# Kernel optimization log

Hardware: AMD Instinct MI355X
Metric: run time of the kernel (lower is better)

## Reference

```python
import jax, jax.numpy as jnp
import numpy as np

ROPE_THETA = 10000.0
N_KV_HEADS = 8


def _rope(x, pos, theta):
    # x: [..., D] with interleaved (even, odd) rotation pairs; pos: scalar position
    D = x.shape[-1]
    freqs = theta ** (-jnp.arange(0, D, 2, dtype=jnp.float32) / D)  # [D/2]
    ang = pos * freqs
    cos, sin = jnp.cos(ang), jnp.sin(ang)
    x1, x2 = x[..., 0::2], x[..., 1::2]
    return jnp.stack([x1 * cos - x2 * sin, x1 * sin + x2 * cos], axis=-1).reshape(x.shape)


def setup_inputs() -> dict:
    key = jax.random.key(0)
    ks = jax.random.split(key, 5)
    B, DIM, CACHE_LEN, HD = 32, 4096, 4096, 128
    N_HEADS = 32
    qkv_out = (N_HEADS + 2 * N_KV_HEADS) * HD  # 6144
    return {
        "x": jax.random.normal(ks[0], (B, DIM), dtype=jnp.float32),
        "cache_k": jax.random.normal(ks[1], (B, CACHE_LEN, N_KV_HEADS, HD), dtype=jnp.float32),
        "cache_v": jax.random.normal(ks[2], (B, CACHE_LEN, N_KV_HEADS, HD), dtype=jnp.float32),
        "wqkv": jax.random.normal(ks[3], (qkv_out, DIM), dtype=jnp.float32) * 0.02,
        "wo": jax.random.normal(ks[4], (DIM, DIM), dtype=jnp.float32) * 0.02,
        "ctx_len": 4095,
    }


def reference(x, cache_k, cache_v, wqkv, wo, ctx_len):
    B = x.shape[0]
    n_kv = cache_k.shape[2]
    hd = cache_k.shape[3]
    n_heads = (wqkv.shape[0] - 2 * n_kv * hd) // hd
    hpg = n_heads // n_kv  # heads per kv group

    # fused QKV projection
    xqkv = x @ wqkv.T  # [B, (n_heads + 2*n_kv)*hd]
    nq = n_heads * hd
    nk = n_kv * hd
    q = xqkv[:, :nq].reshape(B, n_kv, hpg, hd)
    k = xqkv[:, nq:nq + nk].reshape(B, n_kv, hd)
    v = xqkv[:, nq + nk:].reshape(B, n_kv, hd)

    # rope fused with KV-cache write: new token at position ctx_len
    q = _rope(q, ctx_len, ROPE_THETA)
    k = _rope(k, ctx_len, ROPE_THETA)
    cache_k = cache_k.at[:, ctx_len].set(k)
    cache_v = cache_v.at[:, ctx_len].set(v)

    T = ctx_len + 1  # valid cache length (python int -> static slice)
    K = cache_k[:, :T]  # [B, T, n_kv, hd]
    V = cache_v[:, :T]

    # GQA attention: q [b, g, h, d], K/V [b, t, g, d]
    scores = jnp.einsum("bghd,btgd->bght", q, K) / jnp.sqrt(jnp.float32(hd))
    w = jax.nn.softmax(scores, axis=-1)
    o = jnp.einsum("bght,btgd->bghd", w, V).reshape(B, n_heads * hd)
    return o @ wo.T
```

## Files before the change

kernel.cpp:

```cpp
#include <hip/hip_runtime.h>
#include <math.h>

#define BATCH 32
#define DIM   4096
#define CLEN  4096
#define HD    128
#define NKV   8
#define NHEAD 32
#define QKVN  6144
#define KVSTR (NKV * HD)
#define GN    64
#define KSEG  128
#define KSTG  4
#define KTOT  512
#define NSEG  8
#define NCH   16
#define TC    256
#define NSLOT 16
#define MNEG  -1.0e30f
#define SMASK -3.0e38f

template <int CTRL>
__device__ __forceinline__ float dpp_add(float x) {
  int y = __builtin_amdgcn_update_dpp(0, __float_as_int(x), CTRL, 0xF, 0xF, true);
  return x + __int_as_float(y);
}

__device__ __forceinline__ float half_reduce(float s) {
  s = dpp_add<0xB1>(s);
  s = dpp_add<0x4E>(s);
  s = dpp_add<0x124>(s);
  s = dpp_add<0x128>(s);
  s += __int_as_float(__builtin_amdgcn_ds_swizzle(__float_as_int(s), 0x401F));
  return s;
}

__device__ __forceinline__ float xhalf32(float v, int lane) {
  return __int_as_float(__builtin_amdgcn_ds_bpermute((lane ^ 32) << 2, __float_as_int(v)));
}

__global__ __launch_bounds__(256)
void gemm_partial(const float* __restrict__ X, const float* __restrict__ W,
                  float* __restrict__ part, const int N) {
  __shared__ float xs[KSEG * 32];
  __shared__ float wl[KSEG * 64];
  const int tid = threadIdx.x;
  const int c   = tid & 31;
  const int r   = tid >> 5;
  const int cx7 = c & 7;
  const int n0  = blockIdx.x * GN;
  const int k00 = blockIdx.y * KTOT;
  const int bq8 = tid & 7;
  const int tq  = tid >> 3;
  const int nqq = tq >> 1;
  const int nqo = (tq & 1) << 1;

  float a00=0,a01=0, a10=0,a11=0, a20=0,a21=0, a30=0,a31=0;

  float* xwp  = xs + (c * 4) * 32 + ((r ^ cx7) << 2);
  float* wwp0 = wl + (c * 4) * 64 + ((r ^ cx7) << 2);
  float* wwp1 = wwp0 + 32;

  for (int kk = 0; kk < KSTG; ++kk) {
    const int k0 = k00 + kk * KSEG;
    const float* Xp = X + (size_t)(r * 4) * DIM + k0 + c * 4;
    const float4 xv0 = *(const float4*)(Xp);
    const float4 xv1 = *(const float4*)(Xp + DIM);
    const float4 xv2 = *(const float4*)(Xp + 2 * DIM);
    const float4 xv3 = *(const float4*)(Xp + 3 * DIM);
    const float* Wp0 = W + (size_t)(n0 + r * 4) * DIM + k0 + c * 4;
    const float4 wv00 = *(const float4*)(Wp0);
    const float4 wv01 = *(const float4*)(Wp0 + DIM);
    const float4 wv02 = *(const float4*)(Wp0 + 2 * DIM);
    const float4 wv03 = *(const float4*)(Wp0 + 3 * DIM);
    const float* Wp1 = Wp0 + (size_t)32 * DIM;
    const float4 wv10 = *(const float4*)(Wp1);
    const float4 wv11 = *(const float4*)(Wp1 + DIM);
    const float4 wv12 = *(const float4*)(Wp1 + 2 * DIM);
    const float4 wv13 = *(const float4*)(Wp1 + 3 * DIM);

    if (kk) __syncthreads();

    *(float4*)(xwp + 0)   = make_float4(xv0.x, xv1.x, xv2.x, xv3.x);
    *(float4*)(xwp + 32)  = make_float4(xv0.y, xv1.y, xv2.y, xv3.y);
    *(float4*)(xwp + 64)  = make_float4(xv0.z, xv1.z, xv2.z, xv3.z);
    *(float4*)(xwp + 96)  = make_float4(xv0.w, xv1.w, xv2.w, xv3.w);
    *(float4*)(wwp0 + 0)   = make_float4(wv00.x, wv01.x, wv02.x, wv03.x);
    *(float4*)(wwp0 + 64)  = make_float4(wv00.y, wv01.y, wv02.y, wv03.y);
    *(float4*)(wwp0 + 128) = make_float4(wv00.z, wv01.z, wv02.z, wv03.z);
    *(float4*)(wwp0 + 192) = make_float4(wv00.w, wv01.w, wv02.w, wv03.w);
    *(float4*)(wwp1 + 0)   = make_float4(wv10.x, wv11.x, wv12.x, wv13.x);
    *(float4*)(wwp1 + 64)  = make_float4(wv10.y, wv11.y, wv12.y, wv13.y);
    *(float4*)(wwp1 + 128) = make_float4(wv10.z, wv11.z, wv12.z, wv13.z);
    *(float4*)(wwp1 + 192) = make_float4(wv10.w, wv11.w, wv12.w, wv13.w);
    __syncthreads();

#pragma unroll 8
    for (int k2 = 0; k2 < KSEG / 4; ++k2) {
      const int g = k2 & 7;
      const float* xr = xs + (k2 * 4) * 32 + ((bq8 ^ g) << 2);
      const float* wr = wl + (k2 * 4) * 64 + ((nqq ^ g) << 2) + nqo;
#pragma unroll
      for (int j = 0; j < 4; ++j) {
        const float4 xv = *(const float4*)(xr + j * 32);
        const float2 wv = *(const float2*)(wr + j * 64);
        a00 = fmaf(xv.x, wv.x, a00); a01 = fmaf(xv.x, wv.y, a01);
        a10 = fmaf(xv.y, wv.x, a10); a11 = fmaf(xv.y, wv.y, a11);
        a20 = fmaf(xv.z, wv.x, a20); a21 = fmaf(xv.z, wv.y, a21);
        a30 = fmaf(xv.w, wv.x, a30); a31 = fmaf(xv.w, wv.y, a31);
      }
    }
  }
  const int bq = bq8 << 2;
  const int nq = tq << 1;
  float* base = part + ((size_t)blockIdx.y * BATCH + bq) * N + n0 + nq;
  *(float2*)(base)         = make_float2(a00, a01);
  *(float2*)(base + N)     = make_float2(a10, a11);
  *(float2*)(base + 2 * N) = make_float2(a20, a21);
  *(float2*)(base + 3 * N) = make_float2(a30, a31);
}

__global__ __launch_bounds__(256)
void qkv_combine(const float* __restrict__ part, const int* __restrict__ ctxp,
                 float* __restrict__ qw, float* __restrict__ kn, float* __restrict__ vn) {
  const int idx = blockIdx.x * 256 + threadIdx.x;
  const int b  = idx / (QKVN / 2);
  const int c  = idx % (QKVN / 2);
  const int n0 = c * 2;
  float v0 = 0.f, v1 = 0.f;
#pragma unroll
  for (int s = 0; s < NSEG; ++s) {
    const float2 pv = *(const float2*)(part + ((size_t)s * BATCH + b) * QKVN + n0);
    v0 += pv.x; v1 += pv.y;
  }
  const float pos = (float)ctxp[0];
  const float L2T_OVER_64 = 0.20762050593045952f;
  if (n0 < DIM) {
    const int i = (n0 & 127) >> 1;
    const float fr = exp2f(-(float)i * L2T_OVER_64);
    float sn, cs; sincosf(pos * fr, &sn, &cs);
    qw[(size_t)b * DIM + n0]     = v0 * cs - v1 * sn;
    qw[(size_t)b * DIM + n0 + 1] = v0 * sn + v1 * cs;
  } else if (n0 < DIM + NKV * HD) {
    const int nk = n0 - DIM;
    const int i = (nk & 127) >> 1;
    const float fr = exp2f(-(float)i * L2T_OVER_64);
    float sn, cs; sincosf(pos * fr, &sn, &cs);
    kn[(size_t)b * (NKV * HD) + nk]     = v0 * cs - v1 * sn;
    kn[(size_t)b * (NKV * HD) + nk + 1] = v0 * sn + v1 * cs;
  } else {
    const int nv = n0 - DIM - NKV * HD;
    vn[(size_t)b * (NKV * HD) + nv]     = v0;
    vn[(size_t)b * (NKV * HD) + nv + 1] = v1;
  }
}

__device__ __forceinline__ void load8(float4 kb[4], float4 vb[4],
    const float* __restrict__ ckb, const float* __restrict__ cvb,
    const float* __restrict__ knr, const float* __restrict__ vnr,
    const int t0, const int half, const int ctx, const bool edge) {
#pragma unroll
  for (int u = 0; u < 4; ++u) {
    const int tr = t0 + u * 2 + half;
    const float* kp = ckb + (size_t)tr * KVSTR;
    const float* vp = cvb + (size_t)tr * KVSTR;
    if (edge) {
      if (tr == ctx) { kp = knr; vp = vnr; }
    }
    kb[u] = *(const float4*)kp;
    vb[u] = *(const float4*)vp;
  }
}

__device__ __forceinline__ void compute8(const float4 kb[4], const float4 vb[4],
    const float4 q[4], const int t0, const int half, const int ctx, const bool edge,
    float m[4], float l[4], float4 acc[4]) {
#pragma unroll
  for (int u = 0; u < 4; ++u) {
    float s[4];
#pragma unroll
    for (int hh = 0; hh < 4; ++hh) {
      float d = fmaf(kb[u].x, q[hh].x, kb[u].y * q[hh].y);
      d = fmaf(kb[u].z, q[hh].z, d);
      d = fmaf(kb[u].w, q[hh].w, d);
      s[hh] = half_reduce(d);
    }
    if (edge) {
      const int tr = t0 + u * 2 + half;
      if (tr > ctx) { s[0] = SMASK; s[1] = SMASK; s[2] = SMASK; s[3] = SMASK; }
    }
    if ((s[0] > m[0]) | (s[1] > m[1]) | (s[2] > m[2]) | (s[3] > m[3])) {
#pragma unroll
      for (int hh = 0; hh < 4; ++hh) {
        const float mn = fmaxf(m[hh], s[hh]);
        const float rs = __expf(m[hh] - mn);
        l[hh] *= rs;
        acc[hh].x *= rs; acc[hh].y *= rs; acc[hh].z *= rs; acc[hh].w *= rs;
        m[hh] = mn;
      }
    }
#pragma unroll
    for (int hh = 0; hh < 4; ++hh) {
      const float p = __expf(s[hh] - m[hh]);
      l[hh] += p;
      acc[hh].x = fmaf(p, vb[u].x, acc[hh].x);
      acc[hh].y = fmaf(p, vb[u].y, acc[hh].y);
      acc[hh].z = fmaf(p, vb[u].z, acc[hh].z);
      acc[hh].w = fmaf(p, vb[u].w, acc[hh].w);
    }
  }
}

__global__ __launch_bounds__(256)
void attn_fd(const float* __restrict__ qw, const float* __restrict__ knew,
             const float* __restrict__ vnew, const float* __restrict__ ck,
             const float* __restrict__ cv, const int* __restrict__ ctxp,
             float* __restrict__ opart, float* __restrict__ mlp) {
  const int bg   = blockIdx.x;
  const int b = bg >> 3, g = bg & 7;
  const int wid  = threadIdx.x >> 6;
  const int lane = threadIdx.x & 63;
  const int half = lane >> 5;
  const int d4   = (lane & 31) << 2;
  const int cidx = blockIdx.y * 4 + wid;
  const int ctx  = ctxp[0];
  const int c0   = cidx * TC;

  const float sc = 0.08838834764831845f;
  float4 q[4];
#pragma unroll
  for (int hh = 0; hh < 4; ++hh) {
    q[hh] = *(const float4*)(qw + ((size_t)b * NHEAD + g * 4 + hh) * HD + d4);
    q[hh].x *= sc; q[hh].y *= sc; q[hh].z *= sc; q[hh].w *= sc;
  }
  const float* ckb = ck + ((size_t)b * CLEN * NKV + g) * HD + d4;
  const float* cvb = cv + ((size_t)b * CLEN * NKV + g) * HD + d4;
  const float* knr = knew + ((size_t)b * NKV + g) * HD + d4;
  const float* vnr = vnew + ((size_t)b * NKV + g) * HD + d4;

  float m[4] = {MNEG, MNEG, MNEG, MNEG};
  float l[4] = {0.f, 0.f, 0.f, 0.f};
  float4 acc[4] = {};

  float4 ka[4], va[4], kb2[4], vb2[4];
  int t = c0;
  load8(ka, va, ckb, cvb, knr, vnr, t, half, ctx, t + 8 > ctx);
  for (int it = 0; it < TC / 16; ++it) {
    const int tb = t + 8;
    load8(kb2, vb2, ckb, cvb, knr, vnr, tb, half, ctx, tb + 8 > ctx);
    compute8(ka, va, q, t, half, ctx, t + 8 > ctx, m, l, acc);
    const int tn = t + 16;
    if (it + 1 < TC / 16)
      load8(ka, va, ckb, cvb, knr, vnr, tn, half, ctx, tn + 8 > ctx);
    compute8(kb2, vb2, q, tb, half, ctx, tb + 8 > ctx, m, l, acc);
    t = tn;
  }

#pragma unroll
  for (int hh = 0; hh < 4; ++hh) {
    const float mo = xhalf32(m[hh], lane);
    const float lo = xhalf32(l[hh], lane);
    float4 ao;
    ao.x = xhalf32(acc[hh].x, lane); ao.y = xhalf32(acc[hh].y, lane);
    ao.z = xhalf32(acc[hh].z, lane); ao.w = xhalf32(acc[hh].w, lane);
    const float mc = fmaxf(m[hh], mo);
    const float wa = __expf(m[hh] - mc);
    const float wb = __expf(mo - mc);
    l[hh] = wa * l[hh] + wb * lo;
    acc[hh].x = wa * acc[hh].x + wb * ao.x;
    acc[hh].y = wa * acc[hh].y + wb * ao.y;
    acc[hh].z = wa * acc[hh].z + wb * ao.z;
    acc[hh].w = wa * acc[hh].w + wb * ao.w;
    m[hh] = mc;
  }
  if (half == 0) {
#pragma unroll
    for (int hh = 0; hh < 4; ++hh) {
      const int hid = b * NHEAD + g * 4 + hh;
      const size_t slot = (size_t)hid * NSLOT + cidx;
      *(float4*)(opart + slot * HD + d4) = acc[hh];
      if ((lane & 31) == 0) { mlp[slot * 2] = m[hh]; mlp[slot * 2 + 1] = l[hh]; }
    }
  }
}

__global__ __launch_bounds__(128)
void attn_combine(const float* __restrict__ opart, const float* __restrict__ mlp,
                  float* __restrict__ ow) {
  const int p = blockIdx.x;
  const int d = threadIdx.x;
  float M = MNEG;
#pragma unroll
  for (int c = 0; c < NSLOT; ++c) M = fmaxf(M, mlp[((size_t)p * NSLOT + c) * 2]);
  float L = 0.f, O = 0.f;
#pragma unroll 8
  for (int c = 0; c < NSLOT; ++c) {
    const float mi = mlp[((size_t)p * NSLOT + c) * 2];
    const float w = __expf(mi - M);
    L += w * mlp[((size_t)p * NSLOT + c) * 2 + 1];
    O += w * opart[((size_t)p * NSLOT + c) * HD + d];
  }
  ow[(size_t)p * HD + d] = O / L;
}

__global__ __launch_bounds__(256)
void sum_partials(const float* __restrict__ part, float* __restrict__ out,
                  const int total4, const int nseg, const int stride) {
  const int i = blockIdx.x * 256 + threadIdx.x;
  if (i >= total4) return;
  float4 s = make_float4(0.f, 0.f, 0.f, 0.f);
  for (int g = 0; g < nseg; ++g) {
    const float4 v = *(const float4*)(part + (size_t)g * stride + (size_t)i * 4);
    s.x += v.x; s.y += v.y; s.z += v.z; s.w += v.w;
  }
  *(float4*)(out + (size_t)i * 4) = s;
}

extern "C" void kernel_launch(void* const* d_in, const int* in_sizes, int n_in,
                              void* d_out, int out_size, void* d_ws, size_t ws_size,
                              hipStream_t stream) {
  const float* x    = (const float*)d_in[0];
  const float* ck   = (const float*)d_in[1];
  const float* cv   = (const float*)d_in[2];
  const float* wqkv = (const float*)d_in[3];
  const float* wo   = (const float*)d_in[4];
  const int*   ctx  = (const int*)d_in[5];

  float* ws    = (float*)d_ws;
  float* pqkv  = ws;
  float* qw    = pqkv + (size_t)NSEG * BATCH * QKVN;
  float* kn    = qw + (size_t)BATCH * DIM;
  float* vn    = kn + (size_t)BATCH * NKV * HD;
  float* opart = vn + (size_t)BATCH * NKV * HD;
  float* mlp   = opart + (size_t)1024 * NSLOT * HD;
  float* ow    = mlp + (size_t)1024 * NSLOT * 2;
  float* pout  = pqkv;

  gemm_partial<<<dim3(QKVN / GN, NSEG), 256, 0, stream>>>(x, wqkv, pqkv, QKVN);
  qkv_combine<<<dim3(BATCH * QKVN / 2 / 256), 256, 0, stream>>>(pqkv, ctx, qw, kn, vn);
  attn_fd<<<dim3(BATCH * NKV, NCH / 4), 256, 0, stream>>>(qw, kn, vn, ck, cv, ctx, opart, mlp);
  attn_combine<<<dim3(BATCH * NHEAD), HD, 0, stream>>>(opart, mlp, ow);
  gemm_partial<<<dim3(DIM / GN, NSEG), 256, 0, stream>>>(ow, wo, pout, DIM);
  sum_partials<<<dim3((BATCH * DIM / 4 + 255) / 256), 256, 0, stream>>>(
      pout, (float*)d_out, BATCH * DIM / 4, NSEG, BATCH * DIM);
}
```

Before: 269.7 us.

## Prefetch next GEMM K-stage into registers; remap attention so each half-wave owns a KV group

The GEMM now loads the next K-segment of X and W into registers right after the shared-memory barrier, so the global loads overlap the FMA loop over the current segment. The attention kernel is remapped: each block handles one batch and one time chunk, and each half-wave takes a different KV group and walks all rows of the chunk. This removes the cross-half merge via bpermute and exp, and lets one block read full contiguous 4 KB KV rows. In exchange, GEMM register pressure rises, and each half-wave now processes twice as many tokens serially.

Result: slower. 276.5 us (+2.5%).

```diff
diff --git a/kernel.cpp b/kernel.cpp
--- a/kernel.cpp
+++ b/kernel.cpp
@@ -14,7 +14,7 @@
 #define KSTG  4
 #define KTOT  512
 #define NSEG  8
-#define NCH   16
+#define NCHB  16
 #define TC    256
 #define NSLOT 16
 #define MNEG  -1.0e30f
@@ -33,10 +33,6 @@
   s = dpp_add<0x128>(s);
   s += __int_as_float(__builtin_amdgcn_ds_swizzle(__float_as_int(s), 0x401F));
   return s;
-}
-
-__device__ __forceinline__ float xhalf32(float v, int lane) {
-  return __int_as_float(__builtin_amdgcn_ds_bpermute((lane ^ 32) << 2, __float_as_int(v)));
 }
 
 __global__ __launch_bounds__(256)
@@ -61,24 +57,26 @@
   float* wwp0 = wl + (c * 4) * 64 + ((r ^ cx7) << 2);
   float* wwp1 = wwp0 + 32;
 
+  float4 xv0, xv1, xv2, xv3, wv00, wv01, wv02, wv03, wv10, wv11, wv12, wv13;
+  {
+    const float* Xp = X + (size_t)(r * 4) * DIM + k00 + c * 4;
+    xv0 = *(const float4*)(Xp);
+    xv1 = *(const float4*)(Xp + DIM);
+    xv2 = *(const float4*)(Xp + 2 * DIM);
+    xv3 = *(const float4*)(Xp + 3 * DIM);
+    const float* Wp0 = W + (size_t)(n0 + r * 4) * DIM + k00 + c * 4;
+    wv00 = *(const float4*)(Wp0);
+    wv01 = *(const float4*)(Wp0 + DIM);
+    wv02 = *(const float4*)(Wp0 + 2 * DIM);
+    wv03 = *(const float4*)(Wp0 + 3 * DIM);
+    const float* Wp1 = Wp0 + (size_t)32 * DIM;
+    wv10 = *(const float4*)(Wp1);
+    wv11 = *(const float4*)(Wp1 + DIM);
+    wv12 = *(const float4*)(Wp1 + 2 * DIM);
+    wv13 = *(const float4*)(Wp1 + 3 * DIM);
+  }
+
   for (int kk = 0; kk < KSTG; ++kk) {
-    const int k0 = k00 + kk * KSEG;
-    const float* Xp = X + (size_t)(r * 4) * DIM + k0 + c * 4;
-    const float4 xv0 = *(const float4*)(Xp);
-    const float4 xv1 = *(const float4*)(Xp + DIM);
-    const float4 xv2 = *(const float4*)(Xp + 2 * DIM);
-    const float4 xv3 = *(const float4*)(Xp + 3 * DIM);
-    const float* Wp0 = W + (size_t)(n0 + r * 4) * DIM + k0 + c * 4;
-    const float4 wv00 = *(const float4*)(Wp0);
-    const float4 wv01 = *(const float4*)(Wp0 + DIM);
-    const float4 wv02 = *(const float4*)(Wp0 + 2 * DIM);
-    const float4 wv03 = *(const float4*)(Wp0 + 3 * DIM);
-    const float* Wp1 = Wp0 + (size_t)32 * DIM;
-    const float4 wv10 = *(const float4*)(Wp1);
-    const float4 wv11 = *(const float4*)(Wp1 + DIM);
-    const float4 wv12 = *(const float4*)(Wp1 + 2 * DIM);
-    const float4 wv13 = *(const float4*)(Wp1 + 3 * DIM);
-
     if (kk) __syncthreads();
 
     *(float4*)(xwp + 0)   = make_float4(xv0.x, xv1.x, xv2.x, xv3.x);
@@ -94,6 +92,25 @@
     *(float4*)(wwp1 + 128) = make_float4(wv10.z, wv11.z, wv12.z, wv13.z);
     *(float4*)(wwp1 + 192) = make_float4(wv10.w, wv11.w, wv12.w, wv13.w);
     __syncthreads();
+
+    if (kk + 1 < KSTG) {
+      const int k0 = k00 + (kk + 1) * KSEG;
+      const float* Xp = X + (size_t)(r * 4) * DIM + k0 + c * 4;
+      xv0 = *(const float4*)(Xp);
+      xv1 = *(const float4*)(Xp + DIM);
+      xv2 = *(const float4*)(Xp + 2 * DIM);
+      xv3 = *(const float4*)(Xp + 3 * DIM);
+      const float* Wp0 = W + (size_t)(n0 + r * 4) * DIM + k0 + c * 4;
+      wv00 = *(const float4*)(Wp0);
+      wv01 = *(const float4*)(Wp0 + DIM);
+      wv02 = *(const float4*)(Wp0 + 2 * DIM);
+      wv03 = *(const float4*)(Wp0 + 3 * DIM);
+      const float* Wp1 = Wp0 + (size_t)32 * DIM;
+      wv10 = *(const float4*)(Wp1);
+      wv11 = *(const float4*)(Wp1 + DIM);
+      wv12 = *(const float4*)(Wp1 + 2 * DIM);
+      wv13 = *(const float4*)(Wp1 + 3 * DIM);
+    }
 
 #pragma unroll 8
     for (int k2 = 0; k2 < KSEG / 4; ++k2) {
@@ -155,25 +172,25 @@
   }
 }
 
-__device__ __forceinline__ void load8(float4 kb[4], float4 vb[4],
-    const float* __restrict__ ckb, const float* __restrict__ cvb,
+__device__ __forceinline__ void load4(float4 kb[4], float4 vb[4],
+    const float* __restrict__ kbase, const float* __restrict__ vbase,
     const float* __restrict__ knr, const float* __restrict__ vnr,
-    const int t0, const int half, const int ctx, const bool edge) {
+    const int t0, const int ctx, const bool edge) {
 #pragma unroll
   for (int u = 0; u < 4; ++u) {
-    const int tr = t0 + u * 2 + half;
-    const float* kp = ckb + (size_t)tr * KVSTR;
-    const float* vp = cvb + (size_t)tr * KVSTR;
+    const int row = t0 + u;
+    const float* kp = kbase + (size_t)row * KVSTR;
+    const float* vp = vbase + (size_t)row * KVSTR;
     if (edge) {
-      if (tr == ctx) { kp = knr; vp = vnr; }
+      if (row == ctx) { kp = knr; vp = vnr; }
     }
     kb[u] = *(const float4*)kp;
     vb[u] = *(const float4*)vp;
   }
 }
 
-__device__ __forceinline__ void compute8(const float4 kb[4], const float4 vb[4],
-    const float4 q[4], const int t0, const int half, const int ctx, const bool edge,
+__device__ __forceinline__ void compute4(const float4 kb[4], const float4 vb[4],
+    const float4 q[4], const int t0, const int ctx, const bool edge,
     float m[4], float l[4], float4 acc[4]) {
 #pragma unroll
   for (int u = 0; u < 4; ++u) {
@@ -186,8 +203,7 @@
       s[hh] = half_reduce(d);
     }
     if (edge) {
-      const int tr = t0 + u * 2 + half;
-      if (tr > ctx) { s[0] = SMASK; s[1] = SMASK; s[2] = SMASK; s[3] = SMASK; }
+      if (t0 + u > ctx) { s[0] = SMASK; s[1] = SMASK; s[2] = SMASK; s[3] = SMASK; }
     }
     if ((s[0] > m[0]) | (s[1] > m[1]) | (s[2] > m[2]) | (s[3] > m[3])) {
 #pragma unroll
@@ -216,13 +232,13 @@
              const float* __restrict__ vnew, const float* __restrict__ ck,
              const float* __restrict__ cv, const int* __restrict__ ctxp,
              float* __restrict__ opart, float* __restrict__ mlp) {
-  const int bg   = blockIdx.x;
-  const int b = bg >> 3, g = bg & 7;
+  const int b    = blockIdx.x >> 4;
+  const int cidx = blockIdx.x & (NCHB - 1);
   const int wid  = threadIdx.x >> 6;
   const int lane = threadIdx.x & 63;
   const int half = lane >> 5;
+  const int g    = wid * 2 + half;
   const int d4   = (lane & 31) << 2;
-  const int cidx = blockIdx.y * 4 + wid;
   const int ctx  = ctxp[0];
   const int c0   = cidx * TC;
 
@@ -233,54 +249,32 @@
     q[hh] = *(const float4*)(qw + ((size_t)b * NHEAD + g * 4 + hh) * HD + d4);
     q[hh].x *= sc; q[hh].y *= sc; q[hh].z *= sc; q[hh].w *= sc;
   }
-  const float* ckb = ck + ((size_t)b * CLEN * NKV + g) * HD + d4;
-  const float* cvb = cv + ((size_t)b * CLEN * NKV + g) * HD + d4;
-  const float* knr = knew + ((size_t)b * NKV + g) * HD + d4;
-  const float* vnr = vnew + ((size_t)b * NKV + g) * HD + d4;
+  const float* kbase = ck + ((size_t)b * CLEN) * KVSTR + g * HD + d4;
+  const float* vbase = cv + ((size_t)b * CLEN) * KVSTR + g * HD + d4;
+  const float* knr   = knew + ((size_t)b * NKV + g) * HD + d4;
+  const float* vnr   = vnew + ((size_t)b * NKV + g) * HD + d4;
 
   float m[4] = {MNEG, MNEG, MNEG, MNEG};
   float l[4] = {0.f, 0.f, 0.f, 0.f};
   float4 acc[4] = {};
 
-  float4 ka[4], va[4], kb2[4], vb2[4];
-  int t = c0;
-  load8(ka, va, ckb, cvb, knr, vnr, t, half, ctx, t + 8 > ctx);
-  for (int it = 0; it < TC / 16; ++it) {
-    const int tb = t + 8;
-    load8(kb2, vb2, ckb, cvb, knr, vnr, tb, half, ctx, tb + 8 > ctx);
-    compute8(ka, va, q, t, half, ctx, t + 8 > ctx, m, l, acc);
-    const int tn = t + 16;
-    if (it + 1 < TC / 16)
-      load8(ka, va, ckb, cvb, knr, vnr, tn, half, ctx, tn + 8 > ctx);
-    compute8(kb2, vb2, q, tb, half, ctx, tb + 8 > ctx, m, l, acc);
-    t = tn;
+  float4 kA[4], vA[4], kB[4], vB[4];
+  load4(kA, vA, kbase, vbase, knr, vnr, c0, ctx, c0 + 4 > ctx);
+  for (int it = 0; it < TC / 8; ++it) {
+    const int t0 = c0 + it * 8;
+    load4(kB, vB, kbase, vbase, knr, vnr, t0 + 4, ctx, t0 + 8 > ctx);
+    compute4(kA, vA, q, t0, ctx, t0 + 4 > ctx, m, l, acc);
+    if (it + 1 < TC / 8)
+      load4(kA, vA, kbase, vbase, knr, vnr, t0 + 8, ctx, t0 + 12 > ctx);
+    compute4(kB, vB, q, t0 + 4, ctx, t0 + 8 > ctx, m, l, acc);
   }
 
 #pragma unroll
   for (int hh = 0; hh < 4; ++hh) {
-    const float mo = xhalf32(m[hh], lane);
-    const float lo = xhalf32(l[hh], lane);
-    float4 ao;
-    ao.x = xhalf32(acc[hh].x, lane); ao.y = xhalf32(acc[hh].y, lane);
-    ao.z = xhalf32(acc[hh].z, lane); ao.w = xhalf32(acc[hh].w, lane);
-    const float mc = fmaxf(m[hh], mo);
-    const float wa = __expf(m[hh] - mc);
-    const float wb = __expf(mo - mc);
-    l[hh] = wa * l[hh] + wb * lo;
-    acc[hh].x = wa * acc[hh].x + wb * ao.x;
-    acc[hh].y = wa * acc[hh].y + wb * ao.y;
-    acc[hh].z = wa * acc[hh].z + wb * ao.z;
-    acc[hh].w = wa * acc[hh].w + wb * ao.w;
-    m[hh] = mc;
-  }
-  if (half == 0) {
-#pragma unroll
-    for (int hh = 0; hh < 4; ++hh) {
-      const int hid = b * NHEAD + g * 4 + hh;
-      const size_t slot = (size_t)hid * NSLOT + cidx;
-      *(float4*)(opart + slot * HD + d4) = acc[hh];
-      if ((lane & 31) == 0) { mlp[slot * 2] = m[hh]; mlp[slot * 2 + 1] = l[hh]; }
-    }
+    const int hid = b * NHEAD + g * 4 + hh;
+    const size_t slot = (size_t)hid * NSLOT + cidx;
+    *(float4*)(opart + slot * HD + d4) = acc[hh];
+    if ((lane & 31) == 0) { mlp[slot * 2] = m[hh]; mlp[slot * 2 + 1] = l[hh]; }
   }
 }
 
@@ -338,7 +332,7 @@
 
   gemm_partial<<<dim3(QKVN / GN, NSEG), 256, 0, stream>>>(x, wqkv, pqkv, QKVN);
   qkv_combine<<<dim3(BATCH * QKVN / 2 / 256), 256, 0, stream>>>(pqkv, ctx, qw, kn, vn);
-  attn_fd<<<dim3(BATCH * NKV, NCH / 4), 256, 0, stream>>>(qw, kn, vn, ck, cv, ctx, opart, mlp);
+  attn_fd<<<dim3(BATCH * NCHB), 256, 0, stream>>>(qw, kn, vn, ck, cv, ctx, opart, mlp);
   attn_combine<<<dim3(BATCH * NHEAD), HD, 0, stream>>>(opart, mlp, ow);
   gemm_partial<<<dim3(DIM / GN, NSEG), 256, 0, stream>>>(ow, wo, pout, DIM);
   sum_partials<<<dim3((BATCH * DIM / 4 + 255) / 256), 256, 0, stream>>>(
```

## Restructure GEMM partial kernel with 4x4 register tiles and intra-block K split

Applied to the files above, without the earlier changes.

The split-K GEMM now stores X and W tiles row-major in shared memory with an XOR swizzle instead of transposing them. Each thread computes a 4x4 output tile over half of the K segment. The two halves of the block are then reduced through shared memory before the write. This raises the FMA-to-LDS-load ratio (float4 loads feeding 64 FMAs) but adds a shared-memory reduction pass and two extra barriers. The attention kernel only renames variables.

New measurement: 348.4 us. +29.2%, slower.

```diff
diff --git a/kernel.cpp b/kernel.cpp
--- a/kernel.cpp
+++ b/kernel.cpp
@@ -42,82 +42,90 @@
 __global__ __launch_bounds__(256)
 void gemm_partial(const float* __restrict__ X, const float* __restrict__ W,
                   float* __restrict__ part, const int N) {
-  __shared__ float xs[KSEG * 32];
-  __shared__ float wl[KSEG * 64];
-  const int tid = threadIdx.x;
-  const int c   = tid & 31;
-  const int r   = tid >> 5;
-  const int cx7 = c & 7;
-  const int n0  = blockIdx.x * GN;
-  const int k00 = blockIdx.y * KTOT;
-  const int bq8 = tid & 7;
-  const int tq  = tid >> 3;
-  const int nqq = tq >> 1;
-  const int nqo = (tq & 1) << 1;
-
-  float a00=0,a01=0, a10=0,a11=0, a20=0,a21=0, a30=0,a31=0;
-
-  float* xwp  = xs + (c * 4) * 32 + ((r ^ cx7) << 2);
-  float* wwp0 = wl + (c * 4) * 64 + ((r ^ cx7) << 2);
-  float* wwp1 = wwp0 + 32;
+  __shared__ float xs[BATCH * KSEG];
+  __shared__ float wl[GN * KSEG];
+  const int tid  = threadIdx.x;
+  const int cst  = tid & 31;
+  const int rst  = tid >> 5;
+  const int pos  = tid & 127;
+  const int kh   = tid >> 7;
+  const int bsel = pos & 7;
+  const int nsel = pos >> 3;
+  const int n0   = blockIdx.x * GN;
+  const int k00  = blockIdx.y * KTOT;
+
+  float acc[4][4];
+#pragma unroll
+  for (int i = 0; i < 4; ++i)
+#pragma unroll
+    for (int j = 0; j < 4; ++j) acc[i][j] = 0.f;
 
   for (int kk = 0; kk < KSTG; ++kk) {
     const int k0 = k00 + kk * KSEG;
-    const float* Xp = X + (size_t)(r * 4) * DIM + k0 + c * 4;
-    const float4 xv0 = *(const float4*)(Xp);
-    const float4 xv1 = *(const float4*)(Xp + DIM);
-    const float4 xv2 = *(const float4*)(Xp + 2 * DIM);
-    const float4 xv3 = *(const float4*)(Xp + 3 * DIM);
-    const float* Wp0 = W + (size_t)(n0 + r * 4) * DIM + k0 + c * 4;
-    const float4 wv00 = *(const float4*)(Wp0);
-    const float4 wv01 = *(const float4*)(Wp0 + DIM);
-    const float4 wv02 = *(const float4*)(Wp0 + 2 * DIM);
-    const float4 wv03 = *(const float4*)(Wp0 + 3 * DIM);
-    const float* Wp1 = Wp0 + (size_t)32 * DIM;
-    const float4 wv10 = *(const float4*)(Wp1);
-    const float4 wv11 = *(const float4*)(Wp1 + DIM);
-    const float4 wv12 = *(const float4*)(Wp1 + 2 * DIM);
-    const float4 wv13 = *(const float4*)(Wp1 + 3 * DIM);
+    float4 xg[4], wg[8];
+#pragma unroll
+    for (int i = 0; i < 4; ++i)
+      xg[i] = *(const float4*)(X + (size_t)(rst + 8 * i) * DIM + k0 + cst * 4);
+#pragma unroll
+    for (int j = 0; j < 8; ++j)
+      wg[j] = *(const float4*)(W + (size_t)(n0 + rst + 8 * j) * DIM + k0 + cst * 4);
 
     if (kk) __syncthreads();
 
-    *(float4*)(xwp + 0)   = make_float4(xv0.x, xv1.x, xv2.x, xv3.x);
-    *(float4*)(xwp + 32)  = make_float4(xv0.y, xv1.y, xv2.y, xv3.y);
-    *(float4*)(xwp + 64)  = make_float4(xv0.z, xv1.z, xv2.z, xv3.z);
-    *(float4*)(xwp + 96)  = make_float4(xv0.w, xv1.w, xv2.w, xv3.w);
-    *(float4*)(wwp0 + 0)   = make_float4(wv00.x, wv01.x, wv02.x, wv03.x);
-    *(float4*)(wwp0 + 64)  = make_float4(wv00.y, wv01.y, wv02.y, wv03.y);
-    *(float4*)(wwp0 + 128) = make_float4(wv00.z, wv01.z, wv02.z, wv03.z);
-    *(float4*)(wwp0 + 192) = make_float4(wv00.w, wv01.w, wv02.w, wv03.w);
-    *(float4*)(wwp1 + 0)   = make_float4(wv10.x, wv11.x, wv12.x, wv13.x);
-    *(float4*)(wwp1 + 64)  = make_float4(wv10.y, wv11.y, wv12.y, wv13.y);
-    *(float4*)(wwp1 + 128) = make_float4(wv10.z, wv11.z, wv12.z, wv13.z);
-    *(float4*)(wwp1 + 192) = make_float4(wv10.w, wv11.w, wv12.w, wv13.w);
+#pragma unroll
+    for (int i = 0; i < 4; ++i) {
+      const int row = rst + 8 * i;
+      *(float4*)&xs[row * KSEG + ((cst ^ ((row >> 2) & 7)) << 2)] = xg[i];
+    }
+#pragma unroll
+    for (int j = 0; j < 8; ++j) {
+      const int row = rst + 8 * j;
+      *(float4*)&wl[row * KSEG + ((cst ^ ((row >> 2) & 7)) << 2)] = wg[j];
+    }
     __syncthreads();
 
-#pragma unroll 8
-    for (int k2 = 0; k2 < KSEG / 4; ++k2) {
-      const int g = k2 & 7;
-      const float* xr = xs + (k2 * 4) * 32 + ((bq8 ^ g) << 2);
-      const float* wr = wl + (k2 * 4) * 64 + ((nqq ^ g) << 2) + nqo;
-#pragma unroll
-      for (int j = 0; j < 4; ++j) {
-        const float4 xv = *(const float4*)(xr + j * 32);
-        const float2 wv = *(const float2*)(wr + j * 64);
-        a00 = fmaf(xv.x, wv.x, a00); a01 = fmaf(xv.x, wv.y, a01);
-        a10 = fmaf(xv.y, wv.x, a10); a11 = fmaf(xv.y, wv.y, a11);
-        a20 = fmaf(xv.z, wv.x, a20); a21 = fmaf(xv.z, wv.y, a21);
-        a30 = fmaf(xv.w, wv.x, a30); a31 = fmaf(xv.w, wv.y, a31);
-      }
-    }
-  }
-  const int bq = bq8 << 2;
-  const int nq = tq << 1;
-  float* base = part + ((size_t)blockIdx.y * BATCH + bq) * N + n0 + nq;
-  *(float2*)(base)         = make_float2(a00, a01);
-  *(float2*)(base + N)     = make_float2(a10, a11);
-  *(float2*)(base + 2 * N) = make_float2(a20, a21);
-  *(float2*)(base + 3 * N) = make_float2(a30, a31);
+#pragma unroll 4
+    for (int kq16 = 0; kq16 < 16; ++kq16) {
+      const int kq = kh * 16 + kq16;
+      const int xq = (kq ^ bsel) << 2;
+      const int wq = (kq ^ (nsel & 7)) << 2;
+      float4 xv[4], wv[4];
+#pragma unroll
+      for (int j = 0; j < 4; ++j)
+        xv[j] = *(const float4*)&xs[(bsel * 4 + j) * KSEG + xq];
+#pragma unroll
+      for (int j = 0; j < 4; ++j)
+        wv[j] = *(const float4*)&wl[(nsel * 4 + j) * KSEG + wq];
+#pragma unroll
+      for (int bi = 0; bi < 4; ++bi)
+#pragma unroll
+        for (int nj = 0; nj < 4; ++nj) {
+          acc[bi][nj] = fmaf(xv[bi].x, wv[nj].x, acc[bi][nj]);
+          acc[bi][nj] = fmaf(xv[bi].y, wv[nj].y, acc[bi][nj]);
+          acc[bi][nj] = fmaf(xv[bi].z, wv[nj].z, acc[bi][nj]);
+          acc[bi][nj] = fmaf(xv[bi].w, wv[nj].w, acc[bi][nj]);
+        }
+    }
+  }
+
+  __syncthreads();
+  if (kh == 1) {
+#pragma unroll
+    for (int i = 0; i < 4; ++i)
+      *(float4*)&xs[(pos * 4 + i) * 4] =
+          make_float4(acc[i][0], acc[i][1], acc[i][2], acc[i][3]);
+  }
+  __syncthreads();
+  if (kh == 0) {
+#pragma unroll
+    for (int i = 0; i < 4; ++i) {
+      const float4 o = *(const float4*)&xs[(pos * 4 + i) * 4];
+      float4 r = make_float4(acc[i][0] + o.x, acc[i][1] + o.y,
+                             acc[i][2] + o.z, acc[i][3] + o.w);
+      *(float4*)(part + ((size_t)blockIdx.y * BATCH + bsel * 4 + i) * N
+                 + n0 + nsel * 4) = r;
+    }
+  }
 }
 
 __global__ __launch_bounds__(256)
@@ -242,17 +250,17 @@
   float l[4] = {0.f, 0.f, 0.f, 0.f};
   float4 acc[4] = {};
 
-  float4 ka[4], va[4], kb2[4], vb2[4];
+  float4 kA[4], vA[4], kB[4], vB[4];
   int t = c0;
-  load8(ka, va, ckb, cvb, knr, vnr, t, half, ctx, t + 8 > ctx);
+  load8(kA, vA, ckb, cvb, knr, vnr, t, half, ctx, t + 8 > ctx);
   for (int it = 0; it < TC / 16; ++it) {
     const int tb = t + 8;
-    load8(kb2, vb2, ckb, cvb, knr, vnr, tb, half, ctx, tb + 8 > ctx);
-    compute8(ka, va, q, t, half, ctx, t + 8 > ctx, m, l, acc);
+    load8(kB, vB, ckb, cvb, knr, vnr, tb, half, ctx, tb + 8 > ctx);
+    compute8(kA, vA, q, t, half, ctx, t + 8 > ctx, m, l, acc);
     const int tn = t + 16;
     if (it + 1 < TC / 16)
-      load8(ka, va, ckb, cvb, knr, vnr, tn, half, ctx, tn + 8 > ctx);
-    compute8(kb2, vb2, q, tb, half, ctx, tb + 8 > ctx, m, l, acc);
+      load8(kA, vA, ckb, cvb, knr, vnr, tn, half, ctx, tn + 8 > ctx);
+    compute8(kB, vB, q, tb, half, ctx, tb + 8 > ctx, m, l, acc);
     t = tn;
   }
 
```
